# Kernel tuning notes

Hardware: AMD Instinct MI355X
Metric: run time of the kernel (lower is better)

The kernel has to match this reference:

```python
import jax, jax.numpy as jnp
import numpy as np

NUM_GROUPS = 8
EPS = 1e-5


def group_norm(x, scale, bias):
    # x: [b, c, h, w]; 8 groups, affine, eps=1e-5 (torch GroupNorm defaults)
    b, c, h, w = x.shape
    xg = x.reshape(b, NUM_GROUPS, c // NUM_GROUPS * h * w)
    mean = jnp.mean(xg, axis=-1, keepdims=True)
    var = jnp.var(xg, axis=-1, keepdims=True)
    xg = (xg - mean) * jax.lax.rsqrt(var + EPS)
    x = xg.reshape(b, c, h, w)
    return x * scale[None, :, None, None] + bias[None, :, None, None]


def conv1x1(x, w, bias):
    # 1x1 conv == per-pixel linear: x [b,c,h,w], w [c_out,c_in], bias [c_out]
    return jnp.einsum('oc,bchw->bohw', w, x) + bias[None, :, None, None]


def setup_inputs() -> dict:
    key = jax.random.key(0)
    ks = jax.random.split(key, 11)
    b, c, h, w = 8, 512, 32, 32
    init = 1.0 / np.sqrt(c)
    d = {
        'x': jax.random.normal(ks[0], (b, c, h, w), dtype=jnp.float32),
        'gn_scale': jnp.ones((c,), jnp.float32),
        'gn_bias': jnp.zeros((c,), jnp.float32),
        'wq': jax.random.uniform(ks[1], (c, c), jnp.float32, -init, init),
        'bq': jax.random.uniform(ks[2], (c,), jnp.float32, -init, init),
        'wk': jax.random.uniform(ks[3], (c, c), jnp.float32, -init, init),
        'bk': jax.random.uniform(ks[4], (c,), jnp.float32, -init, init),
        'wv': jax.random.uniform(ks[5], (c, c), jnp.float32, -init, init),
        'bv': jax.random.uniform(ks[6], (c,), jnp.float32, -init, init),
        'wproj': jax.random.uniform(ks[7], (c, c), jnp.float32, -init, init),
        'bproj': jax.random.uniform(ks[8], (c,), jnp.float32, -init, init),
    }
    return d


def reference(x, gn_scale, gn_bias, wq, bq, wk, bk, wv, bv, wproj, bproj):
    b, c, h, w = x.shape
    h_ = group_norm(x, gn_scale, gn_bias)
    q = conv1x1(h_, wq, bq).reshape(b, c, h * w)  # [b,c,hw]
    k = conv1x1(h_, wk, bk).reshape(b, c, h * w)
    v = conv1x1(h_, wv, bv).reshape(b, c, h * w)
    scale = 1.0 / np.sqrt(c).astype(np.float32)
    # scores[b,i,j] = sum_c q[b,c,i]*k[b,c,j]
    scores = jnp.einsum('bci,bcj->bij', q, k) * scale
    attn = jax.nn.softmax(scores, axis=2)  # softmax over j (keys)
    # h_[b,c,i] = sum_j v[b,c,j] * attn[b,i,j]
    out = jnp.einsum('bcj,bij->bci', v, attn).reshape(b, c, h, w)
    out = conv1x1(out, wproj, bproj)
    return x + out
```

## Files before the change

### kernel.cpp

```cpp
#include <hip/hip_runtime.h>
#include <hip/hip_bf16.h>

#define DI __device__ __forceinline__

typedef __bf16 bf16x8 __attribute__((ext_vector_type(8)));
typedef float f32x4 __attribute__((ext_vector_type(4)));

typedef const void __attribute__((address_space(1))) gas_t;
typedef void __attribute__((address_space(3))) las_t;

DI unsigned short f2bf(float f) {
    unsigned u = __builtin_bit_cast(unsigned, f);
    u += 0x7fffu + ((u >> 16) & 1u);
    return (unsigned short)(u >> 16);
}

__global__ __launch_bounds__(256) void prep_kernel(const float* __restrict__ x,
                                                   float2* __restrict__ part,
                                                   const float* __restrict__ w0,
                                                   const float* __restrict__ w1,
                                                   const float* __restrict__ w2,
                                                   const float* __restrict__ w3,
                                                   unsigned short* __restrict__ wb) {
    int bx = blockIdx.x;
    int t = threadIdx.x;
    if (bx < 512) {
        int b = bx & 7, g = (bx >> 3) & 7, ch = bx >> 6;
        size_t base = ((size_t)b * 512 + g * 64 + ch * 8) * 1024;
        const float4* xp = (const float4*)(x + base);
        float s = 0.f, q = 0.f;
#pragma unroll
        for (int it = 0; it < 8; ++it) {
            float4 v = xp[it * 256 + t];
            s += (v.x + v.y) + (v.z + v.w);
            q += (v.x * v.x + v.y * v.y) + (v.z * v.z + v.w * v.w);
        }
#pragma unroll
        for (int o = 32; o; o >>= 1) { s += __shfl_xor(s, o); q += __shfl_xor(q, o); }
        __shared__ float rs[4], rq[4];
        int lane = t & 63, wid = t >> 6;
        if (!lane) { rs[wid] = s; rq[wid] = q; }
        __syncthreads();
        if (t == 0)
            part[((b * 8 + g) * 8) + ch] =
                make_float2(rs[0] + rs[1] + rs[2] + rs[3],
                            rq[0] + rq[1] + rq[2] + rq[3]);
    } else {
        int idx4 = bx - 512;
        int w = idx4 >> 8;
        const float* s = (w == 0) ? w0 : (w == 1) ? w1 : (w == 2) ? w2 : w3;
        unsigned short* o = wb + (size_t)w * 262144;
        int idx = (idx4 & 255) * 256 + t;
        float4 v = ((const float4*)s)[idx];
        ushort4 r;
        r.x = f2bf(v.x); r.y = f2bf(v.y); r.z = f2bf(v.z); r.w = f2bf(v.w);
        ((ushort4*)o)[idx] = r;
    }
}

__global__ __launch_bounds__(256) void gn_applyT(const float* __restrict__ x,
                                                 const float2* __restrict__ part,
                                                 const float* __restrict__ gs,
                                                 const float* __restrict__ gb,
                                                 unsigned short* __restrict__ hT) {
    int bx = blockIdx.x;
    int b = bx & 7, g = (bx >> 3) & 7, ic = bx >> 6;
    int bg = b * 8 + g;
    float s = 0.f, q = 0.f;
#pragma unroll
    for (int k = 0; k < 8; ++k) { float2 p = part[bg * 8 + k]; s += p.x; q += p.y; }
    float mean = s * (1.f / 65536.f);
    float var = q * (1.f / 65536.f) - mean * mean;
    float rstd = rsqrtf(var + 1e-5f);

    __shared__ unsigned short tile[128 * 66];
    int t = threadIdx.x;
    int i4 = t & 31, cq = t >> 5;
    size_t xbase = ((size_t)b * 512 + g * 64) * 1024 + ic * 128;
#pragma unroll
    for (int pass = 0; pass < 8; ++pass) {
        int c = pass * 8 + cq;
        float4 v = *(const float4*)&x[xbase + (size_t)c * 1024 + i4 * 4];
        int gc = g * 64 + c;
        float sc = gs[gc] * rstd, bi = gb[gc] - mean * sc;
        unsigned short* tp = &tile[(i4 * 4) * 66 + c];
        tp[0]   = f2bf(v.x * sc + bi);
        tp[66]  = f2bf(v.y * sc + bi);
        tp[132] = f2bf(v.z * sc + bi);
        tp[198] = f2bf(v.w * sc + bi);
    }
    __syncthreads();
    int i = t >> 1, h = t & 1;
    const unsigned short* tp2 = &tile[i * 66 + h * 32];
    unsigned short* op = &hT[(size_t)b * (1024 * 512) + (size_t)(ic * 128 + i) * 512 + g * 64 + h * 32];
#pragma unroll
    for (int cc = 0; cc < 4; ++cc) {
        unsigned short tmp[8];
#pragma unroll
        for (int j = 0; j < 8; ++j) tmp[j] = tp2[cc * 8 + j];
        *(uint4*)&op[cc * 8] = *(const uint4*)tmp;
    }
}

template <int ROWS>
DI void stage_tile(const unsigned short* __restrict__ g, int ldK,
                   unsigned short* lds, int t) {
    int row_in = t >> 3;
    int kg = (t & 7) ^ (row_in & 7);
    const unsigned short* src = g + (size_t)row_in * ldK + kg * 8;
    unsigned short* dst = lds + ((t >> 6) << 9);
#pragma unroll
    for (int c = 0; c < ROWS / 32; ++c) {
        __builtin_amdgcn_global_load_lds(
            (gas_t*)(unsigned long long)(src + (size_t)c * 32 * ldK),
            (las_t*)(unsigned)(unsigned long long)(dst + c * 2048),
            16, 0, 0);
    }
}

DI bf16x8 frag(const unsigned short* lds, int r, int kg) {
    return *(const bf16x8*)((const char*)lds + r * 128 + ((kg ^ (r & 7)) << 4));
}

template <int TM, int MODE, int MINW>
__global__ __launch_bounds__(256, MINW) void gemm_bt(
        const unsigned short* __restrict__ A, const unsigned short* __restrict__ B,
        const float* __restrict__ b0, const float* __restrict__ b1,
        const float* __restrict__ b2,
        void* __restrict__ C0, void* __restrict__ C1, void* __restrict__ C2,
        const float* __restrict__ resid, float* __restrict__ spart,
        int M, int N, int K, float scale, size_t sA, size_t sB, size_t sC) {
    constexpr int MR = TM / 32;
    __shared__ __align__(16) unsigned short As[TM * 64];
    __shared__ __align__(16) unsigned short Bs[128 * 64];
    int bx = blockIdx.x;
    int b = bx & 7;
    int tile = bx >> 3;
    int nTx = N >> 7;
    int tx = tile % nTx, ty = tile / nTx;
    int m0 = ty * TM, n0 = tx << 7;
    const unsigned short* Ag = A + sA * b + (size_t)m0 * K;
    const unsigned short* Bg = B + sB * b + (size_t)n0 * K;
    int t = threadIdx.x;
    int lane = t & 63, wid = t >> 6;
    int wm = (wid >> 1) * (TM / 2), wn = (wid & 1) * 64;
    const int l15 = lane & 15, lks = lane >> 4;

    f32x4 acc[MR][4];
#pragma unroll
    for (int i = 0; i < MR; ++i)
#pragma unroll
        for (int j = 0; j < 4; ++j) acc[i][j] = (f32x4){0.f, 0.f, 0.f, 0.f};

    for (int k0 = 0; k0 < K; k0 += 64) {
        stage_tile<TM>(Ag + k0, K, As, t);
        stage_tile<128>(Bg + k0, K, Bs, t);
        asm volatile("s_waitcnt vmcnt(0)" ::: "memory");
        __syncthreads();
#pragma unroll
        for (int kk = 0; kk < 2; ++kk) {
            bf16x8 a_[MR], b_[4];
#pragma unroll
            for (int m = 0; m < MR; ++m) a_[m] = frag(As, wm + m * 16 + l15, kk * 4 + lks);
#pragma unroll
            for (int n = 0; n < 4; ++n) b_[n] = frag(Bs, wn + n * 16 + l15, kk * 4 + lks);
#pragma unroll
            for (int m = 0; m < MR; ++m)
#pragma unroll
                for (int n = 0; n < 4; ++n)
                    acc[m][n] = __builtin_amdgcn_mfma_f32_16x16x32_bf16(a_[m], b_[n], acc[m][n], 0, 0, 0);
        }
        __syncthreads();
    }

    const int rbase = lks * 4;
    const size_t cb = sC * b;
    if constexpr (MODE == 0) {
        if (m0 < 1024) {
            unsigned short* Ct = (unsigned short*)(m0 < 512 ? C0 : C1) + cb;
            const float* bias = (m0 < 512) ? b0 : b1;
            int moff = (m0 < 512) ? 0 : 512;
#pragma unroll
            for (int m = 0; m < MR; ++m) {
                int mg = m0 - moff + wm + m * 16 + rbase;
                float bv4[4];
#pragma unroll
                for (int j = 0; j < 4; ++j) bv4[j] = bias[mg + j];
#pragma unroll
                for (int n = 0; n < 4; ++n) {
                    int ng = n0 + wn + n * 16 + l15;
                    f32x4 v = acc[m][n];
                    ushort4 o;
                    o.x = f2bf(v[0] + bv4[0]); o.y = f2bf(v[1] + bv4[1]);
                    o.z = f2bf(v[2] + bv4[2]); o.w = f2bf(v[3] + bv4[3]);
                    *(ushort4*)&Ct[(size_t)ng * 512 + mg] = o;
                }
            }
        } else {
            unsigned short* Vb = (unsigned short*)C2 + cb;
#pragma unroll
            for (int m = 0; m < MR; ++m) {
                int mg = m0 - 1024 + wm + m * 16 + rbase;
                float bv4[4];
#pragma unroll
                for (int j = 0; j < 4; ++j) bv4[j] = b2[mg + j];
#pragma unroll
                for (int n = 0; n < 4; ++n) {
                    int ng = n0 + wn + n * 16 + l15;
                    f32x4 v = acc[m][n];
#pragma unroll
                    for (int j = 0; j < 4; ++j)
                        Vb[(size_t)(mg + j) * 1024 + ng] = f2bf(v[j] + bv4[j]);
                }
            }
        }
    } else if constexpr (MODE == 1) {
        unsigned short* Ct = (unsigned short*)C0 + cb;
        float psum[4] = {0.f, 0.f, 0.f, 0.f};
#pragma unroll
        for (int m = 0; m < MR; ++m) {
            int mg = m0 + wm + m * 16 + rbase;
#pragma unroll
            for (int n = 0; n < 4; ++n) {
                int ng = n0 + wn + n * 16 + l15;
                f32x4 v = acc[m][n];
                float e0 = __expf(v[0] * scale), e1 = __expf(v[1] * scale);
                float e2 = __expf(v[2] * scale), e3 = __expf(v[3] * scale);
                psum[n] += (e0 + e1) + (e2 + e3);
                ushort4 o;
                o.x = f2bf(e0); o.y = f2bf(e1); o.z = f2bf(e2); o.w = f2bf(e3);
                *(ushort4*)&Ct[(size_t)ng * M + mg] = o;
            }
        }
        int rb = (m0 >> 7) * 2 + (wid >> 1);
#pragma unroll
        for (int n = 0; n < 4; ++n) {
            float p = psum[n];
            p += __shfl_xor(p, 16);
            p += __shfl_xor(p, 32);
            if (lks == 0) {
                int ng = n0 + wn + n * 16 + l15;
                spart[(size_t)(b * 16 + rb) * 1024 + ng] = p;
            }
        }
    } else if constexpr (MODE == 2) {
        unsigned short* Ct = (unsigned short*)C0 + cb;
        float inv[4];
#pragma unroll
        for (int n = 0; n < 4; ++n) {
            int ng = n0 + wn + n * 16 + l15;
            float ssum = 0.f;
#pragma unroll
            for (int k = 0; k < 16; ++k) ssum += spart[(size_t)(b * 16 + k) * 1024 + ng];
            inv[n] = 1.f / ssum;
        }
#pragma unroll
        for (int m = 0; m < MR; ++m) {
            int mg = m0 + wm + m * 16 + rbase;
#pragma unroll
            for (int n = 0; n < 4; ++n) {
                int ng = n0 + wn + n * 16 + l15;
                f32x4 v = acc[m][n];
                ushort4 o;
                o.x = f2bf(v[0] * inv[n]); o.y = f2bf(v[1] * inv[n]);
                o.z = f2bf(v[2] * inv[n]); o.w = f2bf(v[3] * inv[n]);
                *(ushort4*)&Ct[(size_t)ng * M + mg] = o;
            }
        }
    } else {
        float* Cf = (float*)C0 + cb;
#pragma unroll
        for (int m = 0; m < MR; ++m) {
            int mg = m0 + wm + m * 16 + rbase;
#pragma unroll
            for (int n = 0; n < 4; ++n) {
                int ng = n0 + wn + n * 16 + l15;
                float bn = b0[ng];
                f32x4 v = acc[m][n];
                const float* rp = resid + cb + (size_t)ng * M + mg;
                float4 o;
                o.x = v[0] + bn + rp[0]; o.y = v[1] + bn + rp[1];
                o.z = v[2] + bn + rp[2]; o.w = v[3] + bn + rp[3];
                *(float4*)&Cf[(size_t)ng * M + mg] = o;
            }
        }
    }
}

extern "C" void kernel_launch(void* const* d_in, const int* in_sizes, int n_in,
                              void* d_out, int out_size, void* d_ws, size_t ws_size,
                              hipStream_t stream) {
    const float* x  = (const float*)d_in[0];
    const float* gs = (const float*)d_in[1];
    const float* gb = (const float*)d_in[2];
    const float* wq = (const float*)d_in[3];
    const float* bq = (const float*)d_in[4];
    const float* wk = (const float*)d_in[5];
    const float* bk = (const float*)d_in[6];
    const float* wv = (const float*)d_in[7];
    const float* bv = (const float*)d_in[8];
    const float* wp = (const float*)d_in[9];
    const float* bp = (const float*)d_in[10];
    float* out = (float*)d_out;

    char* ws = (char*)d_ws;
    const size_t MB = 1u << 20;
    unsigned short* hT = (unsigned short*)(ws + 0);
    unsigned short* wb = (unsigned short*)(ws + 8 * MB);
    unsigned short* qT = (unsigned short*)(ws + 10 * MB);
    unsigned short* kT = (unsigned short*)(ws + 18 * MB);
    unsigned short* vN = (unsigned short*)(ws + 26 * MB);
    unsigned short* E  = (unsigned short*)(ws + 34 * MB);
    unsigned short* OT = (unsigned short*)(ws + 50 * MB);
    float2* gnpart     = (float2*)(ws + 58 * MB);
    float*  spart      = (float*)(ws + 58 * MB + 65536);

    const unsigned short* wpb = wb + 3 * 262144;
    const size_t sH = 1024 * 512;
    const size_t sS = 1024 * 1024;

    prep_kernel<<<1536, 256, 0, stream>>>(x, gnpart, wq, wk, wv, wp, wb);
    gn_applyT<<<512, 256, 0, stream>>>(x, gnpart, gs, gb, hT);

    gemm_bt<128, 0, 3><<<96 * 8, 256, 0, stream>>>(
        wb, hT, bq, bk, bv, qT, kT, vN, nullptr, nullptr,
        1536, 1024, 512, 1.f, 0, sH, sH);
    gemm_bt<128, 1, 3><<<64 * 8, 256, 0, stream>>>(
        kT, qT, nullptr, nullptr, nullptr, E, nullptr, nullptr, nullptr, spart,
        1024, 1024, 512, 0.044194173824159216f, sH, sH, sS);
    gemm_bt<64, 2, 3><<<64 * 8, 256, 0, stream>>>(
        vN, E, nullptr, nullptr, nullptr, OT, nullptr, nullptr, nullptr, spart,
        512, 1024, 1024, 1.f, sH, sS, sH);
    gemm_bt<64, 3, 3><<<64 * 8, 256, 0, stream>>>(
        OT, wpb, bp, nullptr, nullptr, out, nullptr, nullptr, x, nullptr,
        1024, 512, 512, 1.f, sH, 0, (size_t)512 * 1024);
}
```

Measured before the change: 80.38 us.

## Double-buffer LDS tiles in attention GEMMs and hoist epilogue loads before main loop

Adds a PIPE template option that double-buffers the A/B LDS tiles, so the next K-slice is loaded asynchronously into the alternate buffer while MFMA runs on the current one. This drops one barrier per iteration. It is enabled for the scores, AV and projection GEMMs, whose min-waves hint drops from 3 to 2 because LDS use doubles. The softmax row-sum inverse and the projection bias are now read before the main loop so their latency overlaps the GEMM. The cost is lower occupancy and more LDS per block.

```diff
diff --git a/kernel.cpp b/kernel.cpp
--- a/kernel.cpp
+++ b/kernel.cpp
@@ -122,7 +122,25 @@
     return *(const bf16x8*)((const char*)lds + r * 128 + ((kg ^ (r & 7)) << 4));
 }
 
-template <int TM, int MODE, int MINW>
+template <int MR>
+DI void compute_step(const unsigned short* As_, const unsigned short* Bs_,
+                     f32x4 (&acc)[MR][4], int wm, int wn, int l15, int lks) {
+#pragma unroll
+    for (int kk = 0; kk < 2; ++kk) {
+        bf16x8 a_[MR], b_[4];
+#pragma unroll
+        for (int m = 0; m < MR; ++m) a_[m] = frag(As_, wm + m * 16 + l15, kk * 4 + lks);
+#pragma unroll
+        for (int n = 0; n < 4; ++n) b_[n] = frag(Bs_, wn + n * 16 + l15, kk * 4 + lks);
+#pragma unroll
+        for (int m = 0; m < MR; ++m)
+#pragma unroll
+            for (int n = 0; n < 4; ++n)
+                acc[m][n] = __builtin_amdgcn_mfma_f32_16x16x32_bf16(a_[m], b_[n], acc[m][n], 0, 0, 0);
+    }
+}
+
+template <int TM, int MODE, int MINW, int PIPE>
 __global__ __launch_bounds__(256, MINW) void gemm_bt(
         const unsigned short* __restrict__ A, const unsigned short* __restrict__ B,
         const float* __restrict__ b0, const float* __restrict__ b1,
@@ -131,8 +149,9 @@
         const float* __restrict__ resid, float* __restrict__ spart,
         int M, int N, int K, float scale, size_t sA, size_t sB, size_t sC) {
     constexpr int MR = TM / 32;
-    __shared__ __align__(16) unsigned short As[TM * 64];
-    __shared__ __align__(16) unsigned short Bs[128 * 64];
+    constexpr int NBUF = PIPE ? 2 : 1;
+    __shared__ __align__(16) unsigned short As[NBUF][TM * 64];
+    __shared__ __align__(16) unsigned short Bs[NBUF][128 * 64];
     int bx = blockIdx.x;
     int b = bx & 7;
     int tile = bx >> 3;
@@ -152,25 +171,50 @@
 #pragma unroll
         for (int j = 0; j < 4; ++j) acc[i][j] = (f32x4){0.f, 0.f, 0.f, 0.f};
 
-    for (int k0 = 0; k0 < K; k0 += 64) {
-        stage_tile<TM>(Ag + k0, K, As, t);
-        stage_tile<128>(Bg + k0, K, Bs, t);
+    float inv[4];
+    if constexpr (MODE == 2) {
+#pragma unroll
+        for (int n = 0; n < 4; ++n) {
+            int ng = n0 + wn + n * 16 + l15;
+            float ssum = 0.f;
+#pragma unroll
+            for (int k = 0; k < 16; ++k) ssum += spart[(size_t)(b * 16 + k) * 1024 + ng];
+            inv[n] = 1.f / ssum;
+        }
+    }
+    float bn4[4];
+    if constexpr (MODE == 3) {
+#pragma unroll
+        for (int n = 0; n < 4; ++n) bn4[n] = b0[n0 + wn + n * 16 + l15];
+    }
+
+    if constexpr (PIPE == 0) {
+        for (int k0 = 0; k0 < K; k0 += 64) {
+            stage_tile<TM>(Ag + k0, K, &As[0][0], t);
+            stage_tile<128>(Bg + k0, K, &Bs[0][0], t);
+            asm volatile("s_waitcnt vmcnt(0)" ::: "memory");
+            __syncthreads();
+            compute_step<MR>(&As[0][0], &Bs[0][0], acc, wm, wn, l15, lks);
+            __syncthreads();
+        }
+    } else {
+        stage_tile<TM>(Ag, K, &As[0][0], t);
+        stage_tile<128>(Bg, K, &Bs[0][0], t);
         asm volatile("s_waitcnt vmcnt(0)" ::: "memory");
         __syncthreads();
-#pragma unroll
-        for (int kk = 0; kk < 2; ++kk) {
-            bf16x8 a_[MR], b_[4];
-#pragma unroll
-            for (int m = 0; m < MR; ++m) a_[m] = frag(As, wm + m * 16 + l15, kk * 4 + lks);
-#pragma unroll
-            for (int n = 0; n < 4; ++n) b_[n] = frag(Bs, wn + n * 16 + l15, kk * 4 + lks);
-#pragma unroll
-            for (int m = 0; m < MR; ++m)
-#pragma unroll
-                for (int n = 0; n < 4; ++n)
-                    acc[m][n] = __builtin_amdgcn_mfma_f32_16x16x32_bf16(a_[m], b_[n], acc[m][n], 0, 0, 0);
-        }
-        __syncthreads();
+        int cur = 0;
+        for (int k0 = 0; k0 < K; k0 += 64) {
+            if (k0 + 64 < K) {
+                stage_tile<TM>(Ag + k0 + 64, K, &As[cur ^ 1][0], t);
+                stage_tile<128>(Bg + k0 + 64, K, &Bs[cur ^ 1][0], t);
+            }
+            compute_step<MR>(&As[cur][0], &Bs[cur][0], acc, wm, wn, l15, lks);
+            if (k0 + 64 < K) {
+                asm volatile("s_waitcnt vmcnt(0)" ::: "memory");
+                __syncthreads();
+            }
+            cur ^= 1;
+        }
     }
 
     const int rbase = lks * 4;
@@ -245,15 +289,6 @@
         }
     } else if constexpr (MODE == 2) {
         unsigned short* Ct = (unsigned short*)C0 + cb;
-        float inv[4];
-#pragma unroll
-        for (int n = 0; n < 4; ++n) {
-            int ng = n0 + wn + n * 16 + l15;
-            float ssum = 0.f;
-#pragma unroll
-            for (int k = 0; k < 16; ++k) ssum += spart[(size_t)(b * 16 + k) * 1024 + ng];
-            inv[n] = 1.f / ssum;
-        }
 #pragma unroll
         for (int m = 0; m < MR; ++m) {
             int mg = m0 + wm + m * 16 + rbase;
@@ -275,12 +310,11 @@
 #pragma unroll
             for (int n = 0; n < 4; ++n) {
                 int ng = n0 + wn + n * 16 + l15;
-                float bn = b0[ng];
                 f32x4 v = acc[m][n];
                 const float* rp = resid + cb + (size_t)ng * M + mg;
                 float4 o;
-                o.x = v[0] + bn + rp[0]; o.y = v[1] + bn + rp[1];
-                o.z = v[2] + bn + rp[2]; o.w = v[3] + bn + rp[3];
+                o.x = v[0] + bn4[n] + rp[0]; o.y = v[1] + bn4[n] + rp[1];
+                o.z = v[2] + bn4[n] + rp[2]; o.w = v[3] + bn4[n] + rp[3];
                 *(float4*)&Cf[(size_t)ng * M + mg] = o;
             }
         }
@@ -322,16 +356,16 @@
     prep_kernel<<<1536, 256, 0, stream>>>(x, gnpart, wq, wk, wv, wp, wb);
     gn_applyT<<<512, 256, 0, stream>>>(x, gnpart, gs, gb, hT);
 
-    gemm_bt<128, 0, 3><<<96 * 8, 256, 0, stream>>>(
+    gemm_bt<128, 0, 3, 0><<<96 * 8, 256, 0, stream>>>(
         wb, hT, bq, bk, bv, qT, kT, vN, nullptr, nullptr,
         1536, 1024, 512, 1.f, 0, sH, sH);
-    gemm_bt<128, 1, 3><<<64 * 8, 256, 0, stream>>>(
+    gemm_bt<128, 1, 2, 1><<<64 * 8, 256, 0, stream>>>(
         kT, qT, nullptr, nullptr, nullptr, E, nullptr, nullptr, nullptr, spart,
         1024, 1024, 512, 0.044194173824159216f, sH, sH, sS);
-    gemm_bt<64, 2, 3><<<64 * 8, 256, 0, stream>>>(
+    gemm_bt<64, 2, 2, 1><<<64 * 8, 256, 0, stream>>>(
         vN, E, nullptr, nullptr, nullptr, OT, nullptr, nullptr, nullptr, spart,
         512, 1024, 1024, 1.f, sH, sS, sH);
-    gemm_bt<64, 3, 3><<<64 * 8, 256, 0, stream>>>(
+    gemm_bt<64, 3, 2, 1><<<64 * 8, 256, 0, stream>>>(
         OT, wpb, bp, nullptr, nullptr, out, nullptr, nullptr, x, nullptr,
         1024, 512, 512, 1.f, sH, 0, (size_t)512 * 1024);
 }
```

Result: faster. 75.79 us (-5.7%).
